# Kernel tuning notes

Hardware: AMD Instinct MI355X
Metric: run time of the kernel (lower is better)

The kernel has to match this reference:

```python
import jax, jax.numpy as jnp
import numpy as np

NUM_E = 50000
EMBED_DIM = 128
HID_DIM = 200
B = 512
N = 50  # candidate_num / history length
ITER_NUM = 3
ALPHA = 0.5
WEIGHT_BASE = 1.0
SQUASH_W = 1.0
SQUASH_EPS = 1e-9
L2_EPS = 1e-12  # torch F.normalize default eps


def setup_inputs() -> dict:
    key = jax.random.key(0)
    k1, k2, k3, k4, k5, k6, k7 = jax.random.split(key, 7)
    idx = jax.random.randint(k1, (B, N), 0, NUM_E)
    times = jax.random.randint(k2, (B, N), 0, 365)
    # embeddings: normal then row-wise L2 normalize (as in init_embeddings)
    emb = jax.random.normal(k3, (NUM_E, EMBED_DIM), dtype=jnp.float32)
    embeddings = emb / jnp.maximum(jnp.linalg.norm(emb, axis=1, keepdims=True), L2_EPS)
    Ws_w = jax.random.normal(k4, (HID_DIM, EMBED_DIM), dtype=jnp.float32) * (2.0 / (HID_DIM + EMBED_DIM)) ** 0.5
    Ws_b = jnp.zeros((HID_DIM,), dtype=jnp.float32)
    mlp_w = jax.random.normal(k5, (NUM_E, HID_DIM), dtype=jnp.float32) * (2.0 / (NUM_E + HID_DIM)) ** 0.5
    mlp_b = jnp.zeros((NUM_E,), dtype=jnp.float32)
    return {"idx": idx, "times": times, "embeddings": embeddings,
            "Ws_w": Ws_w, "Ws_b": Ws_b, "mlp_w": mlp_w, "mlp_b": mlp_b}


def _squash(s):
    # s: [B, H]; squash over last axis (original axis=-2 on [B,1,1,H,1])
    sq = jnp.sum(s * s, axis=-1, keepdims=True)
    scale = sq / (SQUASH_W + sq) / jnp.sqrt(sq + SQUASH_EPS)
    return scale * s


def reference(idx, times, embeddings, Ws_w, Ws_b, mlp_w, mlp_b):
    # gather history embeddings: [B, N, D]
    embeds = embeddings[idx]
    # temporal weighting -> initial routing logits b_ij: [B, N]
    b = (WEIGHT_BASE + 1.0) / (WEIGHT_BASE + times.astype(jnp.float32))
    # Ws linear (dropout is identity at eval): [B, N, H]
    x = jnp.einsum('bnd,hd->bnh', embeds, Ws_w) + Ws_b
    # u_hat: L2-normalized over H
    u_hat = x / jnp.maximum(jnp.linalg.norm(x, axis=-1, keepdims=True), L2_EPS)
    u_det = jax.lax.stop_gradient(u_hat)
    # dynamic routing, fixed ITER_NUM iterations
    for r in range(ITER_NUM):
        c = jax.nn.softmax(b, axis=1) * N            # [B, N]
        s = jnp.einsum('bn,bnh->bh', c, u_hat)       # [B, H]
        v = _squash(s)                               # [B, H]
        if r < ITER_NUM - 1:
            b = b + jnp.einsum('bnh,bh->bn', u_det, v)
    poses, c_ij = v, c                               # [B, H], [B, N]
    # p_ij: scatter-add c_ij per entity id (math of one_hot^T @ c_ij)
    p = jnp.zeros((B, NUM_E), dtype=jnp.float32)
    p = p.at[jnp.arange(B)[:, None], idx].add(c_ij)
    p = jax.nn.softmax(p, axis=1)
    # decoder mlp (reflect=False)
    scores = poses @ mlp_w.T + mlp_b                 # [B, NUM_E]
    sims = jax.nn.softmax(scores, axis=1)
    return jnp.log(ALPHA * p + (1.0 - ALPHA) * sims)
```

## Files before the change

### kernel.cpp

```cpp
#include <hip/hip_runtime.h>
#include <stdint.h>

#define NUM_E 50000
#define EMBED_DIM 128
#define HID_DIM 200
#define BATCH 512
#define NN 50
#define HPAD 208
#define KPAD 224
#define NKT 7
#define NTT2 3136
#define NXB 196

typedef short s16x8 __attribute__((ext_vector_type(8)));
typedef float f32x4 __attribute__((ext_vector_type(4)));

__device__ inline unsigned short f2bf(float f) {
  union { float f; unsigned u; } v; v.f = f;
  unsigned r = v.u + 0x7FFF + ((v.u >> 16) & 1);
  return (unsigned short)(r >> 16);
}
__device__ inline float bf2f(unsigned short b) {
  union { unsigned u; float f; } v; v.u = ((unsigned)b) << 16;
  return v.f;
}

__device__ __forceinline__ void gl_lds16(const unsigned short* g, unsigned short* l) {
  __builtin_amdgcn_global_load_lds(
      (const __attribute__((address_space(1))) unsigned int*)g,
      (__attribute__((address_space(3))) unsigned int*)l, 16, 0, 0);
}

__global__ __launch_bounds__(256) void k_xgemm(
    const int* __restrict__ idx, const float* __restrict__ emb,
    const float* __restrict__ Ws_w, const float* __restrict__ Ws_b,
    unsigned short* __restrict__ x_ws, float* __restrict__ sumsq_ws)
{
  __shared__ unsigned short Al[64 * 40];
  __shared__ unsigned short Bl[208 * 40];
  const int tid = threadIdx.x;
  const int wave = tid >> 6, lane = tid & 63;
  const int q = lane >> 4, l15 = lane & 15;
  const int row0 = blockIdx.x * 64;

  f32x4 acc[13];
  for (int i = 0; i < 13; i++) acc[i] = (f32x4){0, 0, 0, 0};

  for (int kt = 0; kt < 4; ++kt) {
    const int k0 = kt * 32;
    {
      const int r = tid >> 2, q4 = tid & 3;
      const int erow = idx[row0 + r];
      const float* src = emb + (size_t)erow * EMBED_DIM + k0 + q4 * 8;
      float4 f0 = *(const float4*)(src);
      float4 f1 = *(const float4*)(src + 4);
      unsigned short tmp[8] __attribute__((aligned(16))) = {
        f2bf(f0.x), f2bf(f0.y), f2bf(f0.z), f2bf(f0.w),
        f2bf(f1.x), f2bf(f1.y), f2bf(f1.z), f2bf(f1.w)};
      *(uint4*)&Al[r * 40 + q4 * 8] = *(uint4*)tmp;
    }
    if (tid < 208) {
      unsigned short tmp[32] __attribute__((aligned(16)));
      if (tid < HID_DIM) {
        const float* src = Ws_w + (size_t)tid * EMBED_DIM + k0;
        for (int j = 0; j < 8; j++) {
          float4 f = *(const float4*)(src + j * 4);
          tmp[j*4+0] = f2bf(f.x); tmp[j*4+1] = f2bf(f.y);
          tmp[j*4+2] = f2bf(f.z); tmp[j*4+3] = f2bf(f.w);
        }
      } else {
        for (int j = 0; j < 32; j++) tmp[j] = 0;
      }
      for (int j = 0; j < 4; j++)
        *(uint4*)&Bl[tid * 40 + j * 8] = *(uint4*)&tmp[j * 8];
    }
    __syncthreads();
    s16x8 a = *(const s16x8*)&Al[(wave * 16 + l15) * 40 + q * 8];
    for (int ni = 0; ni < 13; ++ni) {
      s16x8 bfr = *(const s16x8*)&Bl[(ni * 16 + l15) * 40 + q * 8];
      acc[ni] = __builtin_amdgcn_mfma_f32_16x16x32_bf16(a, bfr, acc[ni], 0, 0, 0);
    }
    __syncthreads();
  }

  float sq[4] = {0, 0, 0, 0};
  for (int ni = 0; ni < 13; ++ni) {
    const int col = ni * 16 + l15;
    const bool cv = col < HID_DIM;
    const float bias = cv ? Ws_b[col] : 0.f;
    for (int p = 0; p < 4; p++) {
      float v = acc[ni][p] + bias;
      if (cv) sq[p] += v * v;
      const int grow = row0 + wave * 16 + q * 4 + p;
      x_ws[(size_t)grow * HPAD + col] = f2bf(cv ? v : 0.f);
    }
  }
  for (int m = 1; m < 16; m <<= 1)
    for (int p = 0; p < 4; p++) sq[p] += __shfl_xor(sq[p], m, 64);
  if (l15 == 0)
    for (int p = 0; p < 4; p++)
      sumsq_ws[row0 + wave * 16 + q * 4 + p] = sq[p];
}

__global__ __launch_bounds__(256) void k_routing(
    const int* __restrict__ idx, const int* __restrict__ times,
    const unsigned short* __restrict__ x_ws, const float* __restrict__ sumsq_ws,
    unsigned short* __restrict__ Ap, float* __restrict__ poses_f,
    float* __restrict__ expa_ws, float* __restrict__ D_ws)
{
  __shared__ float u[NN * 201];
  __shared__ float cc[NN];
  __shared__ float bb[NN];
  __shared__ float vv[HID_DIM];
  __shared__ float nrm[NN];
  __shared__ int   sidx[NN];
  __shared__ float red[4];
  __shared__ float scaleS;
  const int tid = threadIdx.x;
  const int b = blockIdx.x;

  if (tid < NN) {
    nrm[tid] = fmaxf(sqrtf(sumsq_ws[b * NN + tid]), 1e-12f);
    sidx[tid] = idx[b * NN + tid];
    bb[tid] = 2.0f / (1.0f + (float)times[b * NN + tid]);
  }
  __syncthreads();
  for (int i = tid; i < NN * HID_DIM; i += 256) {
    const int n = i / HID_DIM, h = i - n * HID_DIM;
    u[n * 201 + h] = bf2f(x_ws[(size_t)(b * NN + n) * HPAD + h]) / nrm[n];
  }
  __syncthreads();

  for (int it = 0; it < 3; ++it) {
    if (tid < 64) {
      float x = (tid < NN) ? bb[tid] : -1e30f;
      float m = x;
      for (int d = 1; d < 64; d <<= 1) m = fmaxf(m, __shfl_xor(m, d, 64));
      float e = (tid < NN) ? __expf(x - m) : 0.f;
      float s = e;
      for (int d = 1; d < 64; d <<= 1) s += __shfl_xor(s, d, 64);
      if (tid < NN) cc[tid] = e * (float)NN / s;
    }
    __syncthreads();
    float sh = 0.f;
    if (tid < HID_DIM)
      for (int n = 0; n < NN; n++) sh += cc[n] * u[n * 201 + tid];
    float sq = (tid < HID_DIM) ? sh * sh : 0.f;
    for (int d = 1; d < 64; d <<= 1) sq += __shfl_xor(sq, d, 64);
    if ((tid & 63) == 0) red[tid >> 6] = sq;
    __syncthreads();
    if (tid == 0) {
      const float t = red[0] + red[1] + red[2] + red[3];
      scaleS = t / (1.0f + t) / sqrtf(t + 1e-9f);
    }
    __syncthreads();
    if (tid < HID_DIM) vv[tid] = scaleS * sh;
    __syncthreads();
    if (it < 2) {
      if (tid < NN) {
        float dot = 0.f;
        for (int h = 0; h < HID_DIM; h++) dot += u[tid * 201 + h] * vv[h];
        bb[tid] += dot;
      }
      __syncthreads();
    }
  }
  if (tid < KPAD) {
    const float val = (tid < HID_DIM) ? vv[tid] : 0.f;
    const int kt = tid >> 5, rem = tid & 31, q = rem >> 3, j = rem & 7;
    const int mt = b >> 4, l15 = b & 15;
    Ap[(size_t)(((mt * NKT + kt) * 64) + q * 16 + l15) * 8 + j] = f2bf(val);
  }
  if (tid < HID_DIM) poses_f[b * HID_DIM + tid] = vv[tid];
  if (tid < 64) {
    float a = 0.f; int first = 1;
    const int my = (tid < NN) ? sidx[tid] : -1;
    if (tid < NN) {
      for (int n = 0; n < NN; n++)
        if (sidx[n] == my) { a += cc[n]; if (n < tid) first = 0; }
      expa_ws[b * NN + tid] = __expf(a);
    }
    float contrib = (tid < NN && first) ? (__expf(a) - 1.0f) : 0.f;
    for (int d = 1; d < 64; d <<= 1) contrib += __shfl_xor(contrib, d, 64);
    if (tid == 0) D_ws[b] = (float)NUM_E + contrib;
  }
}

__global__ __launch_bounds__(256) void k_pack(
    const float* __restrict__ mlp_w, unsigned short* __restrict__ Bp)
{
  const int t = blockIdx.x * 256 + threadIdx.x;
  if (t >= NTT2 * NKT * 64) return;
  const int lane = t & 63;
  const int f = t >> 6;
  const int kt = f % NKT;
  const int nt = f / NKT;
  const int n = nt * 16 + (lane & 15);
  const int kb = kt * 32 + (lane >> 4) * 8;
  unsigned short tmp[8] __attribute__((aligned(16)));
  if (n < NUM_E && kb < HID_DIM) {
    const float* src = mlp_w + (size_t)n * HID_DIM + kb;
    float4 f0 = *(const float4*)(src);
    float4 f1 = *(const float4*)(src + 4);
    tmp[0] = f2bf(f0.x); tmp[1] = f2bf(f0.y); tmp[2] = f2bf(f0.z); tmp[3] = f2bf(f0.w);
    tmp[4] = f2bf(f1.x); tmp[5] = f2bf(f1.y); tmp[6] = f2bf(f1.z); tmp[7] = f2bf(f1.w);
  } else {
    for (int j = 0; j < 8; j++) tmp[j] = 0;
  }
  *(uint4*)&Bp[(size_t)t * 8] = *(uint4*)tmp;
}

template<int PASS>
__global__ __launch_bounds__(256, 3) void k_gemm(
    const unsigned short* __restrict__ Ap, const unsigned short* __restrict__ Bp,
    const float* __restrict__ mlp_b, const float* __restrict__ D_ws,
    float* __restrict__ S_ws, float* __restrict__ out)
{
  __shared__ __align__(16) unsigned short As[28 * 512];
  __shared__ __align__(16) unsigned short Bs[16 * 512];
  __shared__ float red[256];
  const int tid = threadIdx.x;
  const int w = tid >> 6, lane = tid & 63;
  const int q = lane >> 4, l15 = lane & 15;
  const int mt0 = blockIdx.y * 4;
  const int m0 = blockIdx.y * 64;
  const int ntb = blockIdx.x * 16 + w * 4;

  #pragma unroll
  for (int i = 0; i < 7; ++i) {
    const int c = w * 7 + i;
    gl_lds16(Ap + ((size_t)mt0 * NKT + c) * 512 + lane * 8, &As[c * 512]);
  }
  if (PASS == 1 && tid < 64) {
    red[tid]      = 0.5f / D_ws[m0 + tid];
    red[64 + tid] = 0.5f / S_ws[m0 + tid];
  }
  float bias[4];
  #pragma unroll
  for (int nl = 0; nl < 4; ++nl) {
    const int col = (ntb + nl) * 16 + l15;
    bias[nl] = (col < NUM_E) ? mlp_b[col] : 0.f;
  }

  f32x4 acc[4][4];
  #pragma unroll
  for (int i = 0; i < 4; i++)
    #pragma unroll
    for (int j = 0; j < 4; j++) acc[i][j] = (f32x4){0, 0, 0, 0};

  for (int kt = 0; kt < NKT; ++kt) {
    #pragma unroll
    for (int nl = 0; nl < 4; ++nl)
      gl_lds16(Bp + ((size_t)(ntb + nl) * NKT + kt) * 512 + lane * 8,
               &Bs[(w * 4 + nl) * 512]);
    __syncthreads();
    s16x8 a[4], bfr[4];
    #pragma unroll
    for (int mi = 0; mi < 4; ++mi)
      a[mi] = *(const s16x8*)&As[((mi * NKT + kt) * 64 + lane) * 8];
    #pragma unroll
    for (int nl = 0; nl < 4; ++nl)
      bfr[nl] = *(const s16x8*)&Bs[((w * 4 + nl) * 64 + lane) * 8];
    #pragma unroll
    for (int nl = 0; nl < 4; ++nl)
      #pragma unroll
      for (int mi = 0; mi < 4; ++mi)
        acc[mi][nl] = __builtin_amdgcn_mfma_f32_16x16x32_bf16(a[mi], bfr[nl], acc[mi][nl], 0, 0, 0);
    __syncthreads();
  }

  if (PASS == 0) {
    float rs[4][4];
    #pragma unroll
    for (int mi = 0; mi < 4; mi++)
      #pragma unroll
      for (int p = 0; p < 4; p++) rs[mi][p] = 0.f;
    #pragma unroll
    for (int mi = 0; mi < 4; ++mi)
      #pragma unroll
      for (int nl = 0; nl < 4; ++nl) {
        const int col = (ntb + nl) * 16 + l15;
        #pragma unroll
        for (int p = 0; p < 4; p++) {
          const float v = acc[mi][nl][p] + bias[nl];
          rs[mi][p] += (col < NUM_E) ? __expf(v) : 0.f;
        }
      }
    #pragma unroll
    for (int m = 1; m < 16; m <<= 1)
      for (int mi = 0; mi < 4; mi++)
        for (int p = 0; p < 4; p++)
          rs[mi][p] += __shfl_xor(rs[mi][p], m, 64);
    if (l15 == 0)
      for (int mi = 0; mi < 4; mi++)
        for (int p = 0; p < 4; p++)
          red[w * 64 + mi * 16 + q * 4 + p] = rs[mi][p];
    __syncthreads();
    if (tid < 64)
      atomicAdd(&S_ws[m0 + tid],
                red[tid] + red[64 + tid] + red[128 + tid] + red[192 + tid]);
  } else {
    #pragma unroll
    for (int mi = 0; mi < 4; ++mi) {
      #pragma unroll
      for (int p = 0; p < 4; p++) {
        const int rl = mi * 16 + q * 4 + p;
        const float invD = red[rl];
        const float invS = red[64 + rl];
        const int row = m0 + rl;
        #pragma unroll
        for (int nl = 0; nl < 4; ++nl) {
          const int col = (ntb + nl) * 16 + l15;
          if (col < NUM_E) {
            const float v = acc[mi][nl][p] + bias[nl];
            out[(size_t)row * NUM_E + col] = __logf(fmaf(__expf(v), invS, invD));
          }
        }
      }
    }
  }
}

__global__ __launch_bounds__(256) void k_fix(
    const int* __restrict__ idx, const float* __restrict__ expa,
    const float* __restrict__ poses_f, const float* __restrict__ mlp_w,
    const float* __restrict__ mlp_b, const float* __restrict__ D_ws,
    const float* __restrict__ S_ws, float* __restrict__ out)
{
  const int t = blockIdx.x * 4 + (threadIdx.x >> 6);
  const int lane = threadIdx.x & 63;
  if (t >= BATCH * NN) return;
  const int b = t / NN;
  const int j = idx[t];
  float dot = 0.f;
  for (int h = lane; h < HID_DIM; h += 64)
    dot += poses_f[b * HID_DIM + h] * mlp_w[(size_t)j * HID_DIM + h];
  for (int m = 1; m < 64; m <<= 1) dot += __shfl_xor(dot, m, 64);
  if (lane == 0) {
    const float s = dot + mlp_b[j];
    out[(size_t)b * NUM_E + j] = __logf(0.5f * expa[t] / D_ws[b] +
                                        0.5f * __expf(s) / S_ws[b]);
  }
}

extern "C" void kernel_launch(void* const* d_in, const int* in_sizes, int n_in,
                              void* d_out, int out_size, void* d_ws, size_t ws_size,
                              hipStream_t stream) {
  const int*   idx   = (const int*)d_in[0];
  const int*   times = (const int*)d_in[1];
  const float* emb   = (const float*)d_in[2];
  const float* Ws_w  = (const float*)d_in[3];
  const float* Ws_b  = (const float*)d_in[4];
  const float* mlp_w = (const float*)d_in[5];
  const float* mlp_b = (const float*)d_in[6];
  float* out = (float*)d_out;

  char* ws = (char*)d_ws;
  unsigned short* Bp    = (unsigned short*)ws; ws += (size_t)NTT2 * NKT * 64 * 8 * 2;
  unsigned short* x_ws  = (unsigned short*)ws; ws += (size_t)BATCH * NN * HPAD * 2;
  unsigned short* Ap    = (unsigned short*)ws; ws += (size_t)32 * NKT * 64 * 8 * 2;
  float* poses_f        = (float*)ws;          ws += (size_t)BATCH * HID_DIM * 4;
  float* sumsq          = (float*)ws;          ws += (size_t)BATCH * NN * 4;
  float* expa           = (float*)ws;          ws += (size_t)BATCH * NN * 4;
  float* D_ws           = (float*)ws;          ws += (size_t)BATCH * 4;
  float* S_ws           = (float*)ws;          ws += (size_t)BATCH * 4;

  hipMemsetAsync(S_ws, 0, BATCH * sizeof(float), stream);
  k_pack   <<<dim3((NTT2 * NKT * 64) / 256), 256, 0, stream>>>(mlp_w, Bp);
  k_xgemm  <<<dim3(400),          256, 0, stream>>>(idx, emb, Ws_w, Ws_b, x_ws, sumsq);
  k_routing<<<dim3(BATCH),        256, 0, stream>>>(idx, times, x_ws, sumsq, Ap, poses_f, expa, D_ws);
  k_gemm<0><<<dim3(NXB, 8),       256, 0, stream>>>(Ap, Bp, mlp_b, D_ws, S_ws, out);
  k_gemm<1><<<dim3(NXB, 8),       256, 0, stream>>>(Ap, Bp, mlp_b, D_ws, S_ws, out);
  k_fix    <<<dim3(BATCH * NN / 4), 256, 0, stream>>>(idx, expa, poses_f, mlp_w, mlp_b, D_ws, S_ws, out);
}
```

Measured before the change: 268.1 us.

## Merge pack, xgemm and memset into one launch; read A fragments directly in GEMM

Folds the mlp_w bf16 packing, the embedding×Ws GEMM and the S_ws zeroing into a single k_prep launch that selects its role by block index. This removes two launches and one memset. The routing kernel now assigns four threads per history row for both the u load and the b update dot product, reducing the latter with shuffles. The score GEMM drops its LDS staging of A, loads A fragments straight from global memory, and raises its occupancy hint to 4 blocks per SM. In exchange it issues repeated global A reads per k-step, and the pack and xgemm blocks now share one grid.

```diff
diff --git a/kernel.cpp b/kernel.cpp
--- a/kernel.cpp
+++ b/kernel.cpp
@@ -11,6 +11,8 @@
 #define NKT 7
 #define NTT2 3136
 #define NXB 196
+#define PACK_BLOCKS 5488
+#define XG_BLOCKS 400
 
 typedef short s16x8 __attribute__((ext_vector_type(8)));
 typedef float f32x4 __attribute__((ext_vector_type(4)));
@@ -31,17 +33,48 @@
       (__attribute__((address_space(3))) unsigned int*)l, 16, 0, 0);
 }
 
-__global__ __launch_bounds__(256) void k_xgemm(
+__global__ __launch_bounds__(256) void k_prep(
     const int* __restrict__ idx, const float* __restrict__ emb,
     const float* __restrict__ Ws_w, const float* __restrict__ Ws_b,
-    unsigned short* __restrict__ x_ws, float* __restrict__ sumsq_ws)
+    const float* __restrict__ mlp_w,
+    unsigned short* __restrict__ Bp, unsigned short* __restrict__ x_ws,
+    float* __restrict__ sumsq_ws, float* __restrict__ S_ws)
 {
   __shared__ unsigned short Al[64 * 40];
   __shared__ unsigned short Bl[208 * 40];
+  const int bx = blockIdx.x;
   const int tid = threadIdx.x;
+
+  if (bx < PACK_BLOCKS) {
+    const int t = bx * 256 + tid;
+    const int lane = t & 63;
+    const int f = t >> 6;
+    const int kt = f % NKT;
+    const int nt = f / NKT;
+    const int n = nt * 16 + (lane & 15);
+    const int kb = kt * 32 + (lane >> 4) * 8;
+    unsigned short tmp[8] __attribute__((aligned(16)));
+    if (n < NUM_E && kb < HID_DIM) {
+      const float* src = mlp_w + (size_t)n * HID_DIM + kb;
+      float4 f0 = *(const float4*)(src);
+      float4 f1 = *(const float4*)(src + 4);
+      tmp[0] = f2bf(f0.x); tmp[1] = f2bf(f0.y); tmp[2] = f2bf(f0.z); tmp[3] = f2bf(f0.w);
+      tmp[4] = f2bf(f1.x); tmp[5] = f2bf(f1.y); tmp[6] = f2bf(f1.z); tmp[7] = f2bf(f1.w);
+    } else {
+      for (int j = 0; j < 8; j++) tmp[j] = 0;
+    }
+    *(uint4*)&Bp[(size_t)t * 8] = *(uint4*)tmp;
+    return;
+  }
+  if (bx >= PACK_BLOCKS + XG_BLOCKS) {
+    S_ws[tid] = 0.f;
+    S_ws[256 + tid] = 0.f;
+    return;
+  }
+
   const int wave = tid >> 6, lane = tid & 63;
   const int q = lane >> 4, l15 = lane & 15;
-  const int row0 = blockIdx.x * 64;
+  const int row0 = (bx - PACK_BLOCKS) * 64;
 
   f32x4 acc[13];
   for (int i = 0; i < 13; i++) acc[i] = (f32x4){0, 0, 0, 0};
@@ -125,9 +158,11 @@
     bb[tid] = 2.0f / (1.0f + (float)times[b * NN + tid]);
   }
   __syncthreads();
-  for (int i = tid; i < NN * HID_DIM; i += 256) {
-    const int n = i / HID_DIM, h = i - n * HID_DIM;
-    u[n * 201 + h] = bf2f(x_ws[(size_t)(b * NN + n) * HPAD + h]) / nrm[n];
+  const int un = tid >> 2, uc0 = (tid & 3) * 50;
+  if (un < NN) {
+    const float inv = 1.0f / nrm[un];
+    const unsigned short* xs = &x_ws[(size_t)(b * NN + un) * HPAD + uc0];
+    for (int j = 0; j < 50; j++) u[un * 201 + uc0 + j] = bf2f(xs[j]) * inv;
   }
   __syncthreads();
 
@@ -157,11 +192,12 @@
     if (tid < HID_DIM) vv[tid] = scaleS * sh;
     __syncthreads();
     if (it < 2) {
-      if (tid < NN) {
-        float dot = 0.f;
-        for (int h = 0; h < HID_DIM; h++) dot += u[tid * 201 + h] * vv[h];
-        bb[tid] += dot;
-      }
+      float d = 0.f;
+      if (un < NN)
+        for (int j = 0; j < 50; j++) d += u[un * 201 + uc0 + j] * vv[uc0 + j];
+      d += __shfl_xor(d, 1, 64);
+      d += __shfl_xor(d, 2, 64);
+      if (un < NN && (tid & 3) == 0) bb[un] += d;
       __syncthreads();
     }
   }
@@ -186,37 +222,12 @@
   }
 }
 
-__global__ __launch_bounds__(256) void k_pack(
-    const float* __restrict__ mlp_w, unsigned short* __restrict__ Bp)
-{
-  const int t = blockIdx.x * 256 + threadIdx.x;
-  if (t >= NTT2 * NKT * 64) return;
-  const int lane = t & 63;
-  const int f = t >> 6;
-  const int kt = f % NKT;
-  const int nt = f / NKT;
-  const int n = nt * 16 + (lane & 15);
-  const int kb = kt * 32 + (lane >> 4) * 8;
-  unsigned short tmp[8] __attribute__((aligned(16)));
-  if (n < NUM_E && kb < HID_DIM) {
-    const float* src = mlp_w + (size_t)n * HID_DIM + kb;
-    float4 f0 = *(const float4*)(src);
-    float4 f1 = *(const float4*)(src + 4);
-    tmp[0] = f2bf(f0.x); tmp[1] = f2bf(f0.y); tmp[2] = f2bf(f0.z); tmp[3] = f2bf(f0.w);
-    tmp[4] = f2bf(f1.x); tmp[5] = f2bf(f1.y); tmp[6] = f2bf(f1.z); tmp[7] = f2bf(f1.w);
-  } else {
-    for (int j = 0; j < 8; j++) tmp[j] = 0;
-  }
-  *(uint4*)&Bp[(size_t)t * 8] = *(uint4*)tmp;
-}
-
 template<int PASS>
-__global__ __launch_bounds__(256, 3) void k_gemm(
+__global__ __launch_bounds__(256, 4) void k_gemm(
     const unsigned short* __restrict__ Ap, const unsigned short* __restrict__ Bp,
     const float* __restrict__ mlp_b, const float* __restrict__ D_ws,
     float* __restrict__ S_ws, float* __restrict__ out)
 {
-  __shared__ __align__(16) unsigned short As[28 * 512];
   __shared__ __align__(16) unsigned short Bs[16 * 512];
   __shared__ float red[256];
   const int tid = threadIdx.x;
@@ -226,11 +237,6 @@
   const int m0 = blockIdx.y * 64;
   const int ntb = blockIdx.x * 16 + w * 4;
 
-  #pragma unroll
-  for (int i = 0; i < 7; ++i) {
-    const int c = w * 7 + i;
-    gl_lds16(Ap + ((size_t)mt0 * NKT + c) * 512 + lane * 8, &As[c * 512]);
-  }
   if (PASS == 1 && tid < 64) {
     red[tid]      = 0.5f / D_ws[m0 + tid];
     red[64 + tid] = 0.5f / S_ws[m0 + tid];
@@ -242,6 +248,8 @@
     bias[nl] = (col < NUM_E) ? mlp_b[col] : 0.f;
   }
 
+  const unsigned short* apBase = Ap + (size_t)mt0 * NKT * 512;
+
   f32x4 acc[4][4];
   #pragma unroll
   for (int i = 0; i < 4; i++)
@@ -253,11 +261,12 @@
     for (int nl = 0; nl < 4; ++nl)
       gl_lds16(Bp + ((size_t)(ntb + nl) * NKT + kt) * 512 + lane * 8,
                &Bs[(w * 4 + nl) * 512]);
-    __syncthreads();
-    s16x8 a[4], bfr[4];
+    s16x8 a[4];
     #pragma unroll
     for (int mi = 0; mi < 4; ++mi)
-      a[mi] = *(const s16x8*)&As[((mi * NKT + kt) * 64 + lane) * 8];
+      a[mi] = *(const s16x8*)&apBase[((mi * NKT + kt) * 64 + lane) * 8];
+    __syncthreads();
+    s16x8 bfr[4];
     #pragma unroll
     for (int nl = 0; nl < 4; ++nl)
       bfr[nl] = *(const s16x8*)&Bs[((w * 4 + nl) * 64 + lane) * 8];
@@ -365,9 +374,8 @@
   float* D_ws           = (float*)ws;          ws += (size_t)BATCH * 4;
   float* S_ws           = (float*)ws;          ws += (size_t)BATCH * 4;
 
-  hipMemsetAsync(S_ws, 0, BATCH * sizeof(float), stream);
-  k_pack   <<<dim3((NTT2 * NKT * 64) / 256), 256, 0, stream>>>(mlp_w, Bp);
-  k_xgemm  <<<dim3(400),          256, 0, stream>>>(idx, emb, Ws_w, Ws_b, x_ws, sumsq);
+  k_prep   <<<dim3(PACK_BLOCKS + XG_BLOCKS + 1), 256, 0, stream>>>(
+      idx, emb, Ws_w, Ws_b, mlp_w, Bp, x_ws, sumsq, S_ws);
   k_routing<<<dim3(BATCH),        256, 0, stream>>>(idx, times, x_ws, sumsq, Ap, poses_f, expa, D_ws);
   k_gemm<0><<<dim3(NXB, 8),       256, 0, stream>>>(Ap, Bp, mlp_b, D_ws, S_ws, out);
   k_gemm<1><<<dim3(NXB, 8),       256, 0, stream>>>(Ap, Bp, mlp_b, D_ws, S_ws, out);
```

Result: no change. 272.2 us (+1.5%).
